# Optimization experiments

Measured on AMD Instinct MI355X. Metric: run time of the kernel, lower is better.

Reference implementation:

```python
import jax, jax.numpy as jnp
import numpy as np

N_NODES = 100000
N_EDGES = 3200000
N_GRAPHS = 1000
IN_DIM = 10
HID = 20
N_CLASSES = 2
BN_EPS = 1e-5


def setup_inputs() -> dict:
    key = jax.random.key(0)
    ks = jax.random.split(key, 12)
    x = jax.random.normal(ks[0], (N_NODES, IN_DIM), dtype=jnp.float32)
    edge_index = jax.random.randint(ks[1], (2, N_EDGES), 0, N_NODES, dtype=jnp.int64)
    batch = jnp.sort(jax.random.randint(ks[2], (N_NODES,), 0, N_GRAPHS, dtype=jnp.int64))
    def lin(k, fan_in, fan_out):
        bound = 1.0 / np.sqrt(fan_in)
        kw, kb = jax.random.split(k)
        W = jax.random.uniform(kw, (fan_in, fan_out), jnp.float32, -bound, bound)
        b = jax.random.uniform(kb, (fan_out,), jnp.float32, -bound, bound)
        return W, b
    W1, b1 = lin(ks[3], IN_DIM, HID)
    W2, b2 = lin(ks[4], HID, HID)
    W3, b3 = lin(ks[5], HID, HID)
    fcW, fcb = lin(ks[6], HID, N_CLASSES)
    ones = jnp.ones((HID,), jnp.float32)
    zeros = jnp.zeros((HID,), jnp.float32)
    return {
        "x": x, "edge_index": edge_index, "batch": batch,
        "W1": W1, "b1": b1, "g1": ones, "beta1": zeros,
        "W2": W2, "b2": b2, "g2": ones, "beta2": zeros,
        "W3": W3, "b3": b3, "g3": ones, "beta3": zeros,
        "fcW": fcW, "fcb": fcb,
    }


def _gin_layer(h, src, dst, W, b, g, beta):
    # GIN aggregation: (1+eps)*x_i + sum_{j->i} x_j, eps = 0
    agg = jax.ops.segment_sum(h[src], dst, num_segments=N_NODES)  # [N, d]
    h = (h + agg) @ W + b                                          # MLP (single Linear)
    mu = jnp.mean(h, axis=0)                                       # BatchNorm (batch stats)
    var = jnp.mean(jnp.square(h - mu), axis=0)
    h = (h - mu) * jax.lax.rsqrt(var + BN_EPS) * g + beta
    return jax.nn.relu(h)                                          # dropout p=0 is identity


def reference(x, edge_index, batch, W1, b1, g1, beta1, W2, b2, g2, beta2,
              W3, b3, g3, beta3, fcW, fcb):
    src, dst = edge_index[0], edge_index[1]
    h = _gin_layer(x, src, dst, W1, b1, g1, beta1)
    h = _gin_layer(h, src, dst, W2, b2, g2, beta2)
    h = _gin_layer(h, src, dst, W3, b3, g3, beta3)
    graph_emb = jax.ops.segment_sum(h, batch, num_segments=N_GRAPHS)  # global add pool
    return graph_emb @ fcW + fcb
```

## Files before the change

kernel.cpp:

```cpp
#include <hip/hip_runtime.h>
#include <hip/hip_bf16.h>

#define N_NODES  100000
#define N_EDGES  3200000
#define N_GRAPHS 1000
#define IN_DIM   10
#define HID      20
#define BN_EPS   1e-5f

#define BSH   7
#define NB    ((N_NODES + 127) / 128)
#define CAP   4608
#define FB    512
#define FT    512
#define FCHUNK ((N_EDGES + FB - 1) / FB)
#define NBG   ((N_NODES + 31) / 32)

__global__ __launch_bounds__(FT) void fill_direct(const int* __restrict__ src,
                                                  const int* __restrict__ dst,
                                                  int* __restrict__ bcur,
                                                  unsigned* __restrict__ packed) {
    __shared__ int sdst[FCHUNK];
    __shared__ int cnt[NB];
    __shared__ int base[NB];
    int t = threadIdx.x;
    for (int i = t; i < NB; i += FT) cnt[i] = 0;
    __syncthreads();
    int e0 = blockIdx.x * FCHUNK;
    int e1 = min(e0 + FCHUNK, N_EDGES);
    int m = e1 - e0;
    for (int i = t; i < m; i += FT) {
        int d = dst[e0 + i];
        sdst[i] = d;
        atomicAdd(&cnt[d >> BSH], 1);
    }
    __syncthreads();
    for (int i = t; i < NB; i += FT) {
        int c = cnt[i];
        base[i] = c ? atomicAdd(&bcur[i], c) : 0;
        cnt[i] = 0;
    }
    __syncthreads();
    for (int i = t; i < m; i += FT) {
        int d = sdst[i];
        int b = d >> BSH;
        int r = atomicAdd(&cnt[b], 1);
        packed[(size_t)b * CAP + base[b] + r] =
            (unsigned)src[e0 + i] | ((unsigned)(d & 127) << 24);
    }
}

__global__ void scan_buckets(const int* __restrict__ bcur, int* __restrict__ off) {
    __shared__ int lds[1024];
    int t = threadIdx.x;
    int v = (t < NB) ? bcur[t] : 0;
    int val = v;
    lds[t] = val; __syncthreads();
    for (int o = 1; o < 1024; o <<= 1) {
        int a = (t >= o) ? lds[t - o] : 0;
        __syncthreads();
        val += a; lds[t] = val;
        __syncthreads();
    }
    if (t < NB) off[t] = val - v;
    if (t == 0) off[NB] = N_EDGES;
}

__global__ __launch_bounds__(512) void sort_bucket(const unsigned* __restrict__ packed,
                                                   const int* __restrict__ bcnt,
                                                   const int* __restrict__ off,
                                                   int* __restrict__ csr,
                                                   int* __restrict__ rp) {
    __shared__ unsigned ebuf[CAP];
    __shared__ int cnt[128];
    __shared__ int cur[128];
    int b = blockIdx.x, t = threadIdx.x;
    int m = bcnt[b];
    int o = off[b];
    const unsigned* pb = packed + (size_t)b * CAP;
    for (int i = t; i < m; i += 512) ebuf[i] = pb[i];
    if (t < 128) cnt[t] = 0;
    __syncthreads();
    for (int i = t; i < m; i += 512) atomicAdd(&cnt[ebuf[i] >> 24], 1);
    __syncthreads();
    int v = 0, val = 0;
    if (t < 128) { v = cnt[t]; val = v; cur[t] = val; }
    __syncthreads();
    for (int ofs = 1; ofs < 128; ofs <<= 1) {
        int add = (t < 128 && t >= ofs) ? cur[t - ofs] : 0;
        __syncthreads();
        if (t < 128) { val += add; cur[t] = val; }
        __syncthreads();
    }
    if (t < 128) {
        int node = b * 128 + t;
        if (node <= N_NODES) rp[node] = o + (val - v);
        cur[t] = val - v;
    }
    __syncthreads();
    for (int i = t; i < m; i += 512) {
        unsigned p = ebuf[i];
        int l = p >> 24;
        int pos = atomicAdd(&cur[l], 1);
        csr[o + pos] = (int)(p & 0xFFFFFFu);
    }
}

template<int DIN, bool BN>
__global__ __launch_bounds__(256) void gather_mlp8(
        const float* __restrict__ h,
        const int* __restrict__ rp, const int* __restrict__ csr,
        const float* __restrict__ W,
        const float* __restrict__ bias,
        const float* __restrict__ ssin,
        float* __restrict__ hpre,
        float* __restrict__ partials)
{
    __shared__ float sW[DIN * HID];
    __shared__ float sb[HID];
    __shared__ float sss[2 * HID];
    __shared__ float red[4][2 * HID];
    int t = threadIdx.x;
    for (int i = t; i < DIN * HID; i += 256) sW[i] = W[i];
    if (t < HID) sb[t] = bias[t];
    if constexpr (BN) { if (t < 2 * HID) sss[t] = ssin[t]; }
    __syncthreads();

    int node = blockIdx.x * 32 + (t >> 3);
    int sub  = t & 7;
    float u[DIN];
#pragma unroll
    for (int k = 0; k < DIN; k++) u[k] = 0.0f;

    auto acc4 = [&](float4 a, int q) {
        float v0 = a.x, v1 = a.y, v2 = a.z, v3 = a.w;
        if constexpr (BN) {
            v0 = fmaxf(fmaf(v0, sss[4*q+0], sss[HID+4*q+0]), 0.f);
            v1 = fmaxf(fmaf(v1, sss[4*q+1], sss[HID+4*q+1]), 0.f);
            v2 = fmaxf(fmaf(v2, sss[4*q+2], sss[HID+4*q+2]), 0.f);
            v3 = fmaxf(fmaf(v3, sss[4*q+3], sss[HID+4*q+3]), 0.f);
        }
        u[4*q] += v0; u[4*q+1] += v1; u[4*q+2] += v2; u[4*q+3] += v3;
    };

    if (node < N_NODES) {
        int e0 = rp[node], e1 = rp[node + 1];
        if (sub == 0) {
            if constexpr (DIN == 20) {
                const float4* hv = (const float4*)(h + (size_t)node * 20);
#pragma unroll
                for (int q = 0; q < 5; q++) acc4(hv[q], q);
            } else {
                const float2* hv = (const float2*)(h + (size_t)node * DIN);
#pragma unroll
                for (int q = 0; q < 5; q++) {
                    float2 a = hv[q];
                    u[2*q] += a.x; u[2*q+1] += a.y;
                }
            }
        }
        int e = e0 + sub;
        if constexpr (DIN == 20) {
            for (; e + 8 < e1; e += 16) {
                int s0 = csr[e], s1 = csr[e + 8];
                const float4* a0 = (const float4*)(h + (size_t)s0 * 20);
                const float4* a1 = (const float4*)(h + (size_t)s1 * 20);
                float4 r0[5], r1[5];
#pragma unroll
                for (int q = 0; q < 5; q++) r0[q] = a0[q];
#pragma unroll
                for (int q = 0; q < 5; q++) r1[q] = a1[q];
#pragma unroll
                for (int q = 0; q < 5; q++) { acc4(r0[q], q); acc4(r1[q], q); }
            }
            if (e < e1) {
                const float4* a0 = (const float4*)(h + (size_t)csr[e] * 20);
#pragma unroll
                for (int q = 0; q < 5; q++) acc4(a0[q], q);
            }
        } else {
            for (; e + 8 < e1; e += 16) {
                int s0 = csr[e], s1 = csr[e + 8];
                const float2* a0 = (const float2*)(h + (size_t)s0 * DIN);
                const float2* a1 = (const float2*)(h + (size_t)s1 * DIN);
                float2 r0[5], r1[5];
#pragma unroll
                for (int q = 0; q < 5; q++) r0[q] = a0[q];
#pragma unroll
                for (int q = 0; q < 5; q++) r1[q] = a1[q];
#pragma unroll
                for (int q = 0; q < 5; q++) {
                    u[2*q]   += r0[q].x + r1[q].x;
                    u[2*q+1] += r0[q].y + r1[q].y;
                }
            }
            if (e < e1) {
                const float2* a0 = (const float2*)(h + (size_t)csr[e] * DIN);
#pragma unroll
                for (int q = 0; q < 5; q++) {
                    float2 x0 = a0[q];
                    u[2*q] += x0.x; u[2*q+1] += x0.y;
                }
            }
        }
    }

#pragma unroll
    for (int k = 0; k < DIN; k++) {
        u[k] += __shfl_xor(u[k], 1);
        u[k] += __shfl_xor(u[k], 2);
        u[k] += __shfl_xor(u[k], 4);
    }

    const int c0 = (sub & 3) * 5;
    float out[5];
#pragma unroll
    for (int j = 0; j < 5; j++) out[j] = sb[c0 + j];
#pragma unroll
    for (int k = 0; k < DIN; k++) {
        float uk = u[k];
#pragma unroll
        for (int j = 0; j < 5; j++)
            out[j] = fmaf(uk, sW[k * HID + c0 + j], out[j]);
    }
    bool live = (node < N_NODES) && (sub < 4);
    if (live) {
        float* op = hpre + (size_t)node * HID + c0;
#pragma unroll
        for (int j = 0; j < 5; j++) op[j] = out[j];
    }

    float msk = live ? 1.0f : 0.0f;
    float s1[5], s2[5];
#pragma unroll
    for (int j = 0; j < 5; j++) {
        float o = out[j] * msk;
        s1[j] = o; s2[j] = o * out[j];
    }
    for (int o = 8; o < 64; o <<= 1) {
#pragma unroll
        for (int j = 0; j < 5; j++) {
            s1[j] += __shfl_down(s1[j], o);
            s2[j] += __shfl_down(s2[j], o);
        }
    }
    int lane = t & 63, wave = t >> 6;
    if (lane < 4) {
#pragma unroll
        for (int j = 0; j < 5; j++) {
            red[wave][lane * 5 + j]       = s1[j];
            red[wave][HID + lane * 5 + j] = s2[j];
        }
    }
    __syncthreads();
    if (t < 2 * HID)
        partials[(size_t)t * NBG + blockIdx.x] =
            red[0][t] + red[1][t] + red[2][t] + red[3][t];
}

__global__ __launch_bounds__(256) void bn_prep(const float* __restrict__ partials,
                                               const float* __restrict__ g,
                                               const float* __restrict__ beta,
                                               float* __restrict__ ss) {
    int c = blockIdx.x, t = threadIdx.x;
    double a1 = 0.0, a2 = 0.0;
    for (int i = t; i < NBG; i += 256) {
        a1 += (double)partials[(size_t)c * NBG + i];
        a2 += (double)partials[(size_t)(c + HID) * NBG + i];
    }
    for (int o = 32; o; o >>= 1) {
        a1 += __shfl_down(a1, o);
        a2 += __shfl_down(a2, o);
    }
    __shared__ double r1[4], r2[4];
    int lane = t & 63, wave = t >> 6;
    if (lane == 0) { r1[wave] = a1; r2[wave] = a2; }
    __syncthreads();
    if (t == 0) {
        double su = r1[0] + r1[1] + r1[2] + r1[3];
        double sq = r2[0] + r2[1] + r2[2] + r2[3];
        double mu  = su / (double)N_NODES;
        double var = sq / (double)N_NODES - mu * mu;
        float sc = g[c] * (float)(1.0 / sqrt(var + (double)BN_EPS));
        ss[c]       = sc;
        ss[HID + c] = beta[c] - (float)mu * sc;
    }
}

__global__ void gptr_kernel(const int* __restrict__ batch, int* __restrict__ gptr) {
    int n = blockIdx.x * blockDim.x + threadIdx.x;
    if (n >= N_NODES) return;
    int g = batch[n];
    int gp = (n == 0) ? -1 : batch[n - 1];
    for (int q = gp + 1; q <= g; q++) gptr[q] = n;
    if (n == N_NODES - 1)
        for (int q = g + 1; q <= N_GRAPHS; q++) gptr[q] = N_NODES;
}

__global__ __launch_bounds__(256) void pool_fc(const float* __restrict__ h,
                                               const int* __restrict__ gptr,
                                               const float* __restrict__ ss,
                                               const float* __restrict__ fcW,
                                               const float* __restrict__ fcb,
                                               float* __restrict__ out) {
    __shared__ float red[12][HID];
    __shared__ float sss[2 * HID];
    __shared__ float pl[HID];
    int g = blockIdx.x, t = threadIdx.x;
    if (t < 2 * HID) sss[t] = ss[t];
    __syncthreads();
    int n0 = gptr[g], n1 = gptr[g + 1];
    if (t < 240) {
        int c = t % HID, grp = t / HID;
        float s = 0.0f;
        for (int n = n0 + grp; n < n1; n += 12) {
            float v = fmaf(h[(size_t)n * HID + c], sss[c], sss[HID + c]);
            s += v > 0.0f ? v : 0.0f;
        }
        red[grp][c] = s;
    }
    __syncthreads();
    if (t < HID) {
        float a = 0.0f;
#pragma unroll
        for (int q = 0; q < 12; q++) a += red[q][t];
        pl[t] = a;
    }
    __syncthreads();
    if (t < 2) {
        float o = fcb[t];
#pragma unroll
        for (int k = 0; k < HID; k++) o = fmaf(pl[k], fcW[k * 2 + t], o);
        out[g * 2 + t] = o;
    }
}

extern "C" void kernel_launch(void* const* d_in, const int* in_sizes, int n_in,
                              void* d_out, int out_size, void* d_ws, size_t ws_size,
                              hipStream_t stream) {
    const float* x     = (const float*)d_in[0];
    const int*   eidx  = (const int*)d_in[1];
    const int*   batch = (const int*)d_in[2];
    const float* W1 = (const float*)d_in[3];
    const float* b1 = (const float*)d_in[4];
    const float* g1 = (const float*)d_in[5];
    const float* be1 = (const float*)d_in[6];
    const float* W2 = (const float*)d_in[7];
    const float* b2 = (const float*)d_in[8];
    const float* g2 = (const float*)d_in[9];
    const float* be2 = (const float*)d_in[10];
    const float* W3 = (const float*)d_in[11];
    const float* b3 = (const float*)d_in[12];
    const float* g3 = (const float*)d_in[13];
    const float* be3 = (const float*)d_in[14];
    const float* fcW = (const float*)d_in[15];
    const float* fcb = (const float*)d_in[16];
    float* out = (float*)d_out;

    const int* src = eidx;
    const int* dst = eidx + N_EDGES;

    char* ws = (char*)d_ws;
    float* hA      = (float*)(ws + 0);
    float* hB      = (float*)(ws + 8000000);
    unsigned* packed = (unsigned*)(ws + 0);
    int*   csr     = (int*)(ws + 16000000);
    int*   rp      = (int*)(ws + 28800000);
    int*   off     = (int*)(ws + 29200128);
    int*   bcur    = (int*)(ws + 29203328);
    float* partials= (float*)(ws + 29209728);
    float* ss1     = (float*)(ws + 29709728);
    float* ss2     = (float*)(ws + 29709888);
    float* ss3     = (float*)(ws + 29710048);
    int*   gptr    = (int*)(ws + 29710208);

    const int BLK = 256;

    hipMemsetAsync(bcur, 0, NB * sizeof(int), stream);
    fill_direct<<<FB, FT, 0, stream>>>(src, dst, bcur, packed);
    scan_buckets<<<1, 1024, 0, stream>>>(bcur, off);
    sort_bucket<<<NB, 512, 0, stream>>>(packed, bcur, off, csr, rp);
    gptr_kernel<<<(N_NODES + BLK - 1) / BLK, BLK, 0, stream>>>(batch, gptr);

    gather_mlp8<IN_DIM, false><<<NBG, BLK, 0, stream>>>(x, rp, csr, W1, b1, ss1, hA, partials);
    bn_prep<<<HID, BLK, 0, stream>>>(partials, g1, be1, ss1);

    gather_mlp8<HID, true><<<NBG, BLK, 0, stream>>>(hA, rp, csr, W2, b2, ss1, hB, partials);
    bn_prep<<<HID, BLK, 0, stream>>>(partials, g2, be2, ss2);

    gather_mlp8<HID, true><<<NBG, BLK, 0, stream>>>(hB, rp, csr, W3, b3, ss2, hA, partials);
    bn_prep<<<HID, BLK, 0, stream>>>(partials, g3, be3, ss3);

    pool_fc<<<N_GRAPHS, BLK, 0, stream>>>(hA, gptr, ss3, fcW, fcb, out);
}
```

Before: 340.2 us.

## Store hidden activations as padded fp16 rows and widen CSR buckets to 256 nodes

Intermediate node features are now written as fp16 with rows padded to 24 halves (48 bytes). Outputs are staged through shared memory so each row goes out as one coalesced store, and layers 2/3 and pooling gather these half-width rows. This cuts random-gather traffic on the edge aggregation, which dominates the runtime. Separately, the bucket sort now uses 256-node buckets and no longer stages dst indices in shared memory, so dst is read twice from global memory. Using fp16 activations adds rounding error, and the statistics are still computed from the fp32 values.

```diff
diff --git a/kernel.cpp b/kernel.cpp
--- a/kernel.cpp
+++ b/kernel.cpp
@@ -1,5 +1,6 @@
 #include <hip/hip_runtime.h>
 #include <hip/hip_bf16.h>
+#include <hip/hip_fp16.h>
 
 #define N_NODES  100000
 #define N_EDGES  3200000
@@ -8,55 +9,50 @@
 #define HID      20
 #define BN_EPS   1e-5f
 
-#define BSH   7
-#define NB    ((N_NODES + 127) / 128)
-#define CAP   4608
+#define BSH   8
+#define NB    ((N_NODES + 255) / 256)
+#define CAP   9216
 #define FB    512
-#define FT    512
 #define FCHUNK ((N_EDGES + FB - 1) / FB)
 #define NBG   ((N_NODES + 31) / 32)
-
-__global__ __launch_bounds__(FT) void fill_direct(const int* __restrict__ src,
-                                                  const int* __restrict__ dst,
-                                                  int* __restrict__ bcur,
-                                                  unsigned* __restrict__ packed) {
-    __shared__ int sdst[FCHUNK];
+#define HS    24
+
+__global__ __launch_bounds__(512) void fill_direct(const int* __restrict__ src,
+                                                   const int* __restrict__ dst,
+                                                   int* __restrict__ bcur,
+                                                   unsigned* __restrict__ packed) {
     __shared__ int cnt[NB];
     __shared__ int base[NB];
     int t = threadIdx.x;
-    for (int i = t; i < NB; i += FT) cnt[i] = 0;
+    for (int i = t; i < NB; i += 512) cnt[i] = 0;
     __syncthreads();
     int e0 = blockIdx.x * FCHUNK;
     int e1 = min(e0 + FCHUNK, N_EDGES);
-    int m = e1 - e0;
-    for (int i = t; i < m; i += FT) {
-        int d = dst[e0 + i];
-        sdst[i] = d;
-        atomicAdd(&cnt[d >> BSH], 1);
-    }
-    __syncthreads();
-    for (int i = t; i < NB; i += FT) {
+    for (int e = e0 + t; e < e1; e += 512)
+        atomicAdd(&cnt[dst[e] >> BSH], 1);
+    __syncthreads();
+    for (int i = t; i < NB; i += 512) {
         int c = cnt[i];
         base[i] = c ? atomicAdd(&bcur[i], c) : 0;
         cnt[i] = 0;
     }
     __syncthreads();
-    for (int i = t; i < m; i += FT) {
-        int d = sdst[i];
+    for (int e = e0 + t; e < e1; e += 512) {
+        int d = dst[e];
         int b = d >> BSH;
         int r = atomicAdd(&cnt[b], 1);
         packed[(size_t)b * CAP + base[b] + r] =
-            (unsigned)src[e0 + i] | ((unsigned)(d & 127) << 24);
+            (unsigned)src[e] | ((unsigned)(d & 255) << 24);
     }
 }
 
 __global__ void scan_buckets(const int* __restrict__ bcur, int* __restrict__ off) {
-    __shared__ int lds[1024];
+    __shared__ int lds[512];
     int t = threadIdx.x;
     int v = (t < NB) ? bcur[t] : 0;
     int val = v;
     lds[t] = val; __syncthreads();
-    for (int o = 1; o < 1024; o <<= 1) {
+    for (int o = 1; o < 512; o <<= 1) {
         int a = (t >= o) ? lds[t - o] : 0;
         __syncthreads();
         val += a; lds[t] = val;
@@ -72,28 +68,28 @@
                                                    int* __restrict__ csr,
                                                    int* __restrict__ rp) {
     __shared__ unsigned ebuf[CAP];
-    __shared__ int cnt[128];
-    __shared__ int cur[128];
+    __shared__ int cnt[256];
+    __shared__ int cur[256];
     int b = blockIdx.x, t = threadIdx.x;
     int m = bcnt[b];
     int o = off[b];
     const unsigned* pb = packed + (size_t)b * CAP;
     for (int i = t; i < m; i += 512) ebuf[i] = pb[i];
-    if (t < 128) cnt[t] = 0;
+    if (t < 256) cnt[t] = 0;
     __syncthreads();
     for (int i = t; i < m; i += 512) atomicAdd(&cnt[ebuf[i] >> 24], 1);
     __syncthreads();
     int v = 0, val = 0;
-    if (t < 128) { v = cnt[t]; val = v; cur[t] = val; }
-    __syncthreads();
-    for (int ofs = 1; ofs < 128; ofs <<= 1) {
-        int add = (t < 128 && t >= ofs) ? cur[t - ofs] : 0;
+    if (t < 256) { v = cnt[t]; val = v; cur[t] = val; }
+    __syncthreads();
+    for (int ofs = 1; ofs < 256; ofs <<= 1) {
+        int add = (t < 256 && t >= ofs) ? cur[t - ofs] : 0;
         __syncthreads();
-        if (t < 128) { val += add; cur[t] = val; }
+        if (t < 256) { val += add; cur[t] = val; }
         __syncthreads();
     }
-    if (t < 128) {
-        int node = b * 128 + t;
+    if (t < 256) {
+        int node = b * 256 + t;
         if (node <= N_NODES) rp[node] = o + (val - v);
         cur[t] = val - v;
     }
@@ -108,18 +104,20 @@
 
 template<int DIN, bool BN>
 __global__ __launch_bounds__(256) void gather_mlp8(
-        const float* __restrict__ h,
+        const float* __restrict__ hf,
+        const __half* __restrict__ hh,
         const int* __restrict__ rp, const int* __restrict__ csr,
         const float* __restrict__ W,
         const float* __restrict__ bias,
         const float* __restrict__ ssin,
-        float* __restrict__ hpre,
+        __half* __restrict__ hout,
         float* __restrict__ partials)
 {
     __shared__ float sW[DIN * HID];
     __shared__ float sb[HID];
     __shared__ float sss[2 * HID];
     __shared__ float red[4][2 * HID];
+    __shared__ __half sh_h[32][HS];
     int t = threadIdx.x;
     for (int i = t; i < DIN * HID; i += 256) sW[i] = W[i];
     if (t < HID) sb[t] = bias[t];
@@ -132,57 +130,70 @@
 #pragma unroll
     for (int k = 0; k < DIN; k++) u[k] = 0.0f;
 
-    auto acc4 = [&](float4 a, int q) {
-        float v0 = a.x, v1 = a.y, v2 = a.z, v3 = a.w;
-        if constexpr (BN) {
-            v0 = fmaxf(fmaf(v0, sss[4*q+0], sss[HID+4*q+0]), 0.f);
-            v1 = fmaxf(fmaf(v1, sss[4*q+1], sss[HID+4*q+1]), 0.f);
-            v2 = fmaxf(fmaf(v2, sss[4*q+2], sss[HID+4*q+2]), 0.f);
-            v3 = fmaxf(fmaf(v3, sss[4*q+3], sss[HID+4*q+3]), 0.f);
-        }
-        u[4*q] += v0; u[4*q+1] += v1; u[4*q+2] += v2; u[4*q+3] += v3;
+    auto accw = [&](const unsigned* w) {
+#pragma unroll
+        for (int q = 0; q < 10; q++) {
+            float2 f = __half22float2(*(const __half2*)&w[q]);
+            float v0 = f.x, v1 = f.y;
+            if constexpr (BN) {
+                v0 = fmaxf(fmaf(v0, sss[2*q+0], sss[HID+2*q+0]), 0.f);
+                v1 = fmaxf(fmaf(v1, sss[2*q+1], sss[HID+2*q+1]), 0.f);
+            }
+            u[2*q] += v0; u[2*q+1] += v1;
+        }
     };
 
     if (node < N_NODES) {
         int e0 = rp[node], e1 = rp[node + 1];
-        if (sub == 0) {
-            if constexpr (DIN == 20) {
-                const float4* hv = (const float4*)(h + (size_t)node * 20);
-#pragma unroll
-                for (int q = 0; q < 5; q++) acc4(hv[q], q);
-            } else {
-                const float2* hv = (const float2*)(h + (size_t)node * DIN);
+        if constexpr (DIN == 20) {
+            if (sub == 0) {
+                const __half* r = hh + (size_t)node * HS;
+                unsigned w[10];
+                uint4 A = *(const uint4*)r;
+                uint4 B = *(const uint4*)(r + 8);
+                uint2 C = *(const uint2*)(r + 16);
+                w[0]=A.x; w[1]=A.y; w[2]=A.z; w[3]=A.w;
+                w[4]=B.x; w[5]=B.y; w[6]=B.z; w[7]=B.w;
+                w[8]=C.x; w[9]=C.y;
+                accw(w);
+            }
+            int e = e0 + sub;
+            for (; e + 8 < e1; e += 16) {
+                int s0 = csr[e], s1 = csr[e + 8];
+                const __half* r0 = hh + (size_t)s0 * HS;
+                const __half* r1 = hh + (size_t)s1 * HS;
+                uint4 A0 = *(const uint4*)r0;
+                uint4 B0 = *(const uint4*)(r0 + 8);
+                uint2 C0 = *(const uint2*)(r0 + 16);
+                uint4 A1 = *(const uint4*)r1;
+                uint4 B1 = *(const uint4*)(r1 + 8);
+                uint2 C1 = *(const uint2*)(r1 + 16);
+                unsigned w0[10] = {A0.x,A0.y,A0.z,A0.w,B0.x,B0.y,B0.z,B0.w,C0.x,C0.y};
+                unsigned w1[10] = {A1.x,A1.y,A1.z,A1.w,B1.x,B1.y,B1.z,B1.w,C1.x,C1.y};
+                accw(w0); accw(w1);
+            }
+            if (e < e1) {
+                const __half* r0 = hh + (size_t)csr[e] * HS;
+                uint4 A = *(const uint4*)r0;
+                uint4 B = *(const uint4*)(r0 + 8);
+                uint2 C = *(const uint2*)(r0 + 16);
+                unsigned w[10] = {A.x,A.y,A.z,A.w,B.x,B.y,B.z,B.w,C.x,C.y};
+                accw(w);
+            }
+        } else {
+            if (sub == 0) {
+                const float2* hv = (const float2*)(hf + (size_t)node * DIN);
 #pragma unroll
                 for (int q = 0; q < 5; q++) {
                     float2 a = hv[q];
                     u[2*q] += a.x; u[2*q+1] += a.y;
                 }
             }
-        }
-        int e = e0 + sub;
-        if constexpr (DIN == 20) {
+            int e = e0 + sub;
             for (; e + 8 < e1; e += 16) {
                 int s0 = csr[e], s1 = csr[e + 8];
-                const float4* a0 = (const float4*)(h + (size_t)s0 * 20);
-                const float4* a1 = (const float4*)(h + (size_t)s1 * 20);
-                float4 r0[5], r1[5];
-#pragma unroll
-                for (int q = 0; q < 5; q++) r0[q] = a0[q];
-#pragma unroll
-                for (int q = 0; q < 5; q++) r1[q] = a1[q];
-#pragma unroll
-                for (int q = 0; q < 5; q++) { acc4(r0[q], q); acc4(r1[q], q); }
-            }
-            if (e < e1) {
-                const float4* a0 = (const float4*)(h + (size_t)csr[e] * 20);
-#pragma unroll
-                for (int q = 0; q < 5; q++) acc4(a0[q], q);
-            }
-        } else {
-            for (; e + 8 < e1; e += 16) {
-                int s0 = csr[e], s1 = csr[e + 8];
-                const float2* a0 = (const float2*)(h + (size_t)s0 * DIN);
-                const float2* a1 = (const float2*)(h + (size_t)s1 * DIN);
+                const float2* a0 = (const float2*)(hf + (size_t)s0 * DIN);
+                const float2* a1 = (const float2*)(hf + (size_t)s1 * DIN);
                 float2 r0[5], r1[5];
 #pragma unroll
                 for (int q = 0; q < 5; q++) r0[q] = a0[q];
@@ -195,7 +206,7 @@
                 }
             }
             if (e < e1) {
-                const float2* a0 = (const float2*)(h + (size_t)csr[e] * DIN);
+                const float2* a0 = (const float2*)(hf + (size_t)csr[e] * DIN);
 #pragma unroll
                 for (int q = 0; q < 5; q++) {
                     float2 x0 = a0[q];
@@ -225,9 +236,9 @@
     }
     bool live = (node < N_NODES) && (sub < 4);
     if (live) {
-        float* op = hpre + (size_t)node * HID + c0;
-#pragma unroll
-        for (int j = 0; j < 5; j++) op[j] = out[j];
+        int nl = t >> 3;
+#pragma unroll
+        for (int j = 0; j < 5; j++) sh_h[nl][c0 + j] = __float2half(out[j]);
     }
 
     float msk = live ? 1.0f : 0.0f;
@@ -253,6 +264,17 @@
         }
     }
     __syncthreads();
+    if (t < 32) {
+        int n2 = blockIdx.x * 32 + t;
+        if (n2 < N_NODES) {
+            const uint4* sp = (const uint4*)&sh_h[t][0];
+            uint4 a0 = sp[0], a1 = sp[1];
+            uint2 a2 = ((const uint2*)sp)[4];
+            uint4* gp = (uint4*)(hout + (size_t)n2 * HS);
+            gp[0] = a0; gp[1] = a1;
+            ((uint2*)gp)[4] = a2;
+        }
+    }
     if (t < 2 * HID)
         partials[(size_t)t * NBG + blockIdx.x] =
             red[0][t] + red[1][t] + red[2][t] + red[3][t];
@@ -297,7 +319,7 @@
         for (int q = g + 1; q <= N_GRAPHS; q++) gptr[q] = N_NODES;
 }
 
-__global__ __launch_bounds__(256) void pool_fc(const float* __restrict__ h,
+__global__ __launch_bounds__(256) void pool_fc(const __half* __restrict__ h,
                                                const int* __restrict__ gptr,
                                                const float* __restrict__ ss,
                                                const float* __restrict__ fcW,
@@ -314,7 +336,7 @@
         int c = t % HID, grp = t / HID;
         float s = 0.0f;
         for (int n = n0 + grp; n < n1; n += 12) {
-            float v = fmaf(h[(size_t)n * HID + c], sss[c], sss[HID + c]);
+            float v = fmaf(__half2float(h[(size_t)n * HS + c]), sss[c], sss[HID + c]);
             s += v > 0.0f ? v : 0.0f;
         }
         red[grp][c] = s;
@@ -361,8 +383,8 @@
     const int* dst = eidx + N_EDGES;
 
     char* ws = (char*)d_ws;
-    float* hA      = (float*)(ws + 0);
-    float* hB      = (float*)(ws + 8000000);
+    __half* hA16   = (__half*)(ws + 0);
+    __half* hB16   = (__half*)(ws + 4800000);
     unsigned* packed = (unsigned*)(ws + 0);
     int*   csr     = (int*)(ws + 16000000);
     int*   rp      = (int*)(ws + 28800000);
@@ -377,19 +399,22 @@
     const int BLK = 256;
 
     hipMemsetAsync(bcur, 0, NB * sizeof(int), stream);
-    fill_direct<<<FB, FT, 0, stream>>>(src, dst, bcur, packed);
-    scan_buckets<<<1, 1024, 0, stream>>>(bcur, off);
+    fill_direct<<<FB, 512, 0, stream>>>(src, dst, bcur, packed);
+    scan_buckets<<<1, 512, 0, stream>>>(bcur, off);
     sort_bucket<<<NB, 512, 0, stream>>>(packed, bcur, off, csr, rp);
     gptr_kernel<<<(N_NODES + BLK - 1) / BLK, BLK, 0, stream>>>(batch, gptr);
 
-    gather_mlp8<IN_DIM, false><<<NBG, BLK, 0, stream>>>(x, rp, csr, W1, b1, ss1, hA, partials);
+    gather_mlp8<IN_DIM, false><<<NBG, BLK, 0, stream>>>(x, (const __half*)nullptr,
+        rp, csr, W1, b1, ss1, hA16, partials);
     bn_prep<<<HID, BLK, 0, stream>>>(partials, g1, be1, ss1);
 
-    gather_mlp8<HID, true><<<NBG, BLK, 0, stream>>>(hA, rp, csr, W2, b2, ss1, hB, partials);
+    gather_mlp8<HID, true><<<NBG, BLK, 0, stream>>>((const float*)nullptr, hA16,
+        rp, csr, W2, b2, ss1, hB16, partials);
     bn_prep<<<HID, BLK, 0, stream>>>(partials, g2, be2, ss2);
 
-    gather_mlp8<HID, true><<<NBG, BLK, 0, stream>>>(hB, rp, csr, W3, b3, ss2, hA, partials);
+    gather_mlp8<HID, true><<<NBG, BLK, 0, stream>>>((const float*)nullptr, hB16,
+        rp, csr, W3, b3, ss2, hA16, partials);
     bn_prep<<<HID, BLK, 0, stream>>>(partials, g3, be3, ss3);
 
-    pool_fc<<<N_GRAPHS, BLK, 0, stream>>>(hA, gptr, ss3, fcW, fcb, out);
-}
+    pool_fc<<<N_GRAPHS, BLK, 0, stream>>>(hA16, gptr, ss3, fcW, fcb, out);
+}
```

New measurement: 317.1 us. 1.07x faster.
